# Kernel tuning notes

Measured on AMD Instinct MI355X. Metric: run time of the kernel, lower is better.

Reference implementation:

```python
import jax, jax.numpy as jnp
import numpy as np

EPS = 1e-8
N_ITER = 3
S = 8      # n_slots
D = 64     # slot_size
HID = 128  # mlp hidden


def _ln(x, w, b):
    m = jnp.mean(x, axis=-1, keepdims=True)
    v = jnp.var(x, axis=-1, keepdims=True)
    return (x - m) * jax.lax.rsqrt(v + 1e-5) * w + b


def setup_inputs() -> dict:
    key = jax.random.key(0)
    ks = jax.random.split(key, 20)
    B, N, Din = 128, 4096, 64
    g = lambda k, sh, s: (jax.random.normal(k, sh, jnp.float32) * s)
    return {
        "inputs": jax.random.normal(ks[0], (B, N, Din), jnp.float32),
        "eps_noise": jax.random.normal(ks[1], (B, S, D), jnp.float32),
        "slot_mu": g(ks[2], (1, 1, D), 0.1),
        "slot_logvar": g(ks[3], (1, 1, D), 0.1),
        "k_w": g(ks[4], (D, Din), 1.0 / np.sqrt(Din)),
        "v_w": g(ks[5], (D, Din), 1.0 / np.sqrt(Din)),
        "q_w": g(ks[6], (D, D), 1.0 / np.sqrt(D)),
        "ni_w": jnp.ones((Din,), jnp.float32), "ni_b": jnp.zeros((Din,), jnp.float32),
        "ns_w": jnp.ones((D,), jnp.float32),  "ns_b": jnp.zeros((D,), jnp.float32),
        "nr_w": jnp.ones((D,), jnp.float32),  "nr_b": jnp.zeros((D,), jnp.float32),
        "gru_wih": g(ks[7], (3 * D, D), 1.0 / np.sqrt(D)),
        "gru_whh": g(ks[8], (3 * D, D), 1.0 / np.sqrt(D)),
        "gru_bih": jnp.zeros((3 * D,), jnp.float32),
        "gru_bhh": jnp.zeros((3 * D,), jnp.float32),
        "mlp_w1": g(ks[9], (HID, D), 1.0 / np.sqrt(D)),
        "mlp_w2": g(ks[10], (D, HID), 1.0 / np.sqrt(HID)),
        "mlp_b2": jnp.zeros((D,), jnp.float32),
    }


def _gru(x, h, wih, whh, bih, bhh):
    gi = x @ wih.T + bih  # [BS, 3D]
    gh = h @ whh.T + bhh
    i_r, i_z, i_n = jnp.split(gi, 3, axis=-1)
    h_r, h_z, h_n = jnp.split(gh, 3, axis=-1)
    r = jax.nn.sigmoid(i_r + h_r)
    z = jax.nn.sigmoid(i_z + h_z)
    n = jnp.tanh(i_n + r * h_n)
    return (1.0 - z) * n + z * h


def _step(slots, k, v, q_w, ns_w, ns_b, nr_w, nr_b,
          gru_wih, gru_whh, gru_bih, gru_bhh, mlp_w1, mlp_w2, mlp_b2):
    B = slots.shape[0]
    q = _ln(slots, ns_w, ns_b) @ q_w.T                     # [B,S,D]
    logits = jnp.einsum('bnd,bsd->bns', k, q)              # [B,N,S]
    w = jax.nn.softmax(logits, axis=-1) + EPS              # softmax over slots
    w = w / jnp.sum(w, axis=-2, keepdims=True)             # renorm over tokens
    atten_maps = jnp.einsum('bns,bnd->bsd', w, v)          # [B,S,D]
    h = _gru(atten_maps.reshape(B * S, D), slots.reshape(B * S, D),
             gru_wih, gru_whh, gru_bih, gru_bhh)
    h = h + (jax.nn.relu(_ln(h, nr_w, nr_b) @ mlp_w1.T) @ mlp_w2.T + mlp_b2)
    return h.reshape(B, S, D), w


def reference(inputs, eps_noise, slot_mu, slot_logvar, k_w, v_w, q_w,
              ni_w, ni_b, ns_w, ns_b, nr_w, nr_b,
              gru_wih, gru_whh, gru_bih, gru_bhh, mlp_w1, mlp_w2, mlp_b2):
    std = jnp.exp(0.5 * slot_logvar)
    slots = slot_mu + std * eps_noise                      # [B,S,D]
    x = _ln(inputs, ni_w, ni_b)
    k = (x @ k_w.T) / np.sqrt(D).astype(np.float32)        # [B,N,D]
    v = x @ v_w.T
    args = (q_w, ns_w, ns_b, nr_w, nr_b, gru_wih, gru_whh,
            gru_bih, gru_bhh, mlp_w1, mlp_w2, mlp_b2)
    for _ in range(N_ITER):
        slots, w = _step(slots, k, v, *args)
    slots, w = _step(jax.lax.stop_gradient(slots), k, v, *args)
    return slots, w
```

## Files before the change

### kernel.cpp

```cpp
#include <hip/hip_runtime.h>
#include <hip/hip_bf16.h>

#define BB 128
#define NN 4096
#define DD 64
#define SS 8
#define HH 128

typedef __attribute__((ext_vector_type(8))) short short8;
typedef __attribute__((ext_vector_type(4))) float f32x4;

__device__ __forceinline__ float warp_red_sum(float v) {
    #pragma unroll
    for (int off = 32; off; off >>= 1) v += __shfl_xor(v, off);
    return v;
}

__device__ __forceinline__ float bcastlane(float v, int l) {
    return __int_as_float(__builtin_amdgcn_readlane(__float_as_int(v), l));
}

__device__ __forceinline__ unsigned short bfu(float f) {
    __hip_bfloat16 h = __float2bfloat16(f);
    return *(unsigned short*)&h;
}

__device__ __forceinline__ unsigned pk2(float a, float b) {
    return (unsigned)bfu(a) | ((unsigned)bfu(b) << 16);
}

__global__ __launch_bounds__(256) void prep_kernel(
    const float* __restrict__ v_w, const float* __restrict__ q_w,
    const float* __restrict__ wih, const float* __restrict__ whh,
    const float* __restrict__ w1, const float* __restrict__ w2,
    float* __restrict__ vwT, float* __restrict__ qwT,
    float* __restrict__ wihT, float* __restrict__ whhT,
    float* __restrict__ w1T, float* __restrict__ w2T)
{
    int i0 = blockIdx.x * blockDim.x + threadIdx.x;
    int nthr = gridDim.x * blockDim.x;
    for (int t = i0; t < 4096; t += nthr) {
        int i = t >> 6, o = t & 63;
        vwT[t] = v_w[o * 64 + i];
        qwT[t] = q_w[o * 64 + i];
    }
    for (int t = i0; t < 12288; t += nthr) {
        int r = t / 192, c = t % 192;
        wihT[t] = wih[c * 64 + r];
        whhT[t] = whh[c * 64 + r];
    }
    for (int t = i0; t < 8192; t += nthr) {
        int r = t >> 7, c = t & 127;
        w1T[t] = w1[c * 64 + r];
    }
    for (int t = i0; t < 8192; t += nthr) {
        int r = t >> 6, c = t & 63;
        w2T[t] = w2[c * 128 + r];
    }
}

__global__ __launch_bounds__(256) void init_q_kernel(
    const float* __restrict__ eps, const float* __restrict__ mu,
    const float* __restrict__ lv, const float* __restrict__ qwT,
    const float* __restrict__ k_w,
    const float* __restrict__ nsw, const float* __restrict__ nsb,
    float* __restrict__ slots, unsigned short* __restrict__ qb,
    float* __restrict__ zbuf)
{
    const int tid = threadIdx.x, lane = tid & 63;
    const int row = blockIdx.x * 4 + (tid >> 6);
    const int idx = row * 64 + lane;
    float s0 = mu[lane] + __expf(0.5f * lv[lane]) * eps[idx];
    slots[idx] = s0;
    float m = warp_red_sum(s0) * (1.0f / 64.0f);
    float dx = s0 - m;
    float var = warp_red_sum(dx * dx) * (1.0f / 64.0f);
    float xln = dx * rsqrtf(var + 1e-5f) * nsw[lane] + nsb[lane];
    float q = 0.f;
    #pragma unroll 8
    for (int i = 0; i < 64; ++i) q = fmaf(bcastlane(xln, i), qwT[i * 64 + lane], q);
    float qp = 0.f;
    #pragma unroll 8
    for (int o = 0; o < 64; ++o) qp = fmaf(bcastlane(q, o), k_w[o * 64 + lane], qp);
    qb[idx] = bfu(qp * 0.125f);
    int g = blockIdx.x * 256 + tid;
    for (int j = g; j < 66560; j += 65536) zbuf[j] = 0.f;
}

__global__ __launch_bounds__(256) void phase_a_ln(
    const float* __restrict__ inp, const float* __restrict__ niw, const float* __restrict__ nib,
    unsigned short* __restrict__ xb, unsigned short* __restrict__ xbt)
{
    __shared__ unsigned short xt[64 * 136];
    const int tid = threadIdx.x, lane = tid & 63, widx = tid >> 6;
    const int t8 = lane >> 3, d8 = lane & 7;
    const float4 wn0 = *(const float4*)&niw[d8 * 8];
    const float4 wn1 = *(const float4*)&niw[d8 * 8 + 4];
    const float4 bn0 = *(const float4*)&nib[d8 * 8];
    const float4 bn1 = *(const float4*)&nib[d8 * 8 + 4];
    const int tok0 = blockIdx.x * 128;
    #pragma unroll
    for (int it = 0; it < 4; ++it) {
        const int m = widx * 32 + it * 8 + t8;
        const float* rowp = inp + (size_t)(tok0 + m) * 64 + d8 * 8;
        float4 a = *(const float4*)rowp;
        float4 c = *(const float4*)(rowp + 4);
        float s1 = (a.x + a.y + a.z + a.w) + (c.x + c.y + c.z + c.w);
        float s2 = fmaf(a.x, a.x, fmaf(a.y, a.y, fmaf(a.z, a.z, a.w * a.w)));
        s2 = fmaf(c.x, c.x, fmaf(c.y, c.y, fmaf(c.z, c.z, fmaf(c.w, c.w, s2))));
        #pragma unroll
        for (int o = 1; o < 8; o <<= 1) { s1 += __shfl_xor(s1, o); s2 += __shfl_xor(s2, o); }
        float mean = s1 * (1.0f / 64.0f);
        float var = s2 * (1.0f / 64.0f) - mean * mean;
        float rstd = rsqrtf(var + 1e-5f);
        float y[8];
        y[0] = (a.x - mean) * rstd * wn0.x + bn0.x;
        y[1] = (a.y - mean) * rstd * wn0.y + bn0.y;
        y[2] = (a.z - mean) * rstd * wn0.z + bn0.z;
        y[3] = (a.w - mean) * rstd * wn0.w + bn0.w;
        y[4] = (c.x - mean) * rstd * wn1.x + bn1.x;
        y[5] = (c.y - mean) * rstd * wn1.y + bn1.y;
        y[6] = (c.z - mean) * rstd * wn1.z + bn1.z;
        y[7] = (c.w - mean) * rstd * wn1.w + bn1.w;
        uint4 o4;
        o4.x = pk2(y[0], y[1]); o4.y = pk2(y[2], y[3]);
        o4.z = pk2(y[4], y[5]); o4.w = pk2(y[6], y[7]);
        *(uint4*)&xb[(size_t)(tok0 + m) * 64 + d8 * 8] = o4;
        const int mh = m >> 3, ml = m & 7;
        #pragma unroll
        for (int j = 0; j < 8; ++j) {
            const int d = d8 * 8 + j;
            const int col = (((mh ^ ((d >> 2) & 15)) << 3) | ml);
            xt[d * 136 + col] = bfu(y[j]);
        }
    }
    __syncthreads();
    const int b = blockIdx.x >> 5, tin = (blockIdx.x & 31) * 128;
    const int d = tid >> 2, q4 = tid & 3;
    const int sr = (d >> 2) & 15;
    #pragma unroll
    for (int c = 0; c < 4; ++c) {
        const int cc = q4 * 4 + c;
        uint4 o = *(uint4*)&xt[d * 136 + ((cc ^ sr) << 3)];
        *(uint4*)&xbt[((size_t)b * 64 + d) * 4096 + tin + cc * 8] = o;
    }
}

__global__ __launch_bounds__(256) void attn_mfma(
    const __hip_bfloat16* __restrict__ xb, const unsigned short* __restrict__ xbt,
    const unsigned short* __restrict__ qb,
    float* __restrict__ numer, float* __restrict__ denom, float* __restrict__ wout)
{
    __shared__ unsigned short smem[5760];
    unsigned short* Qs = smem;
    const int tid = threadIdx.x, lane = tid & 63, widx = tid >> 6;
    unsigned short* wls = smem + 1152 + widx * 1152;
    const int b = blockIdx.y;

    for (int t = tid; t < 1024; t += 256) {
        int s = t >> 6, dd = t & 63;
        Qs[s * 72 + dd] = (s < 8) ? qb[b * 512 + t] : (unsigned short)0;
    }
    for (int t = lane; t < 576; t += 64) wls[576 + t] = 0;
    __syncthreads();

    const int quad = lane >> 4, l16 = lane & 15;
    short8 aq0 = *(const short8*)&Qs[l16 * 72 + quad * 8];
    short8 aq1 = *(const short8*)&Qs[l16 * 72 + 32 + quad * 8];

    f32x4 accv[4];
    #pragma unroll
    for (int nt = 0; nt < 4; ++nt) accv[nt] = (f32x4){0.f, 0.f, 0.f, 0.f};
    float dacc[4] = {0.f, 0.f, 0.f, 0.f};

    const int twave0 = blockIdx.x * 512 + widx * 128;
    #pragma unroll
    for (int iter = 0; iter < 2; ++iter) {
        const int t0 = twave0 + iter * 64;
        short8 bvr[8];
        #pragma unroll
        for (int ks = 0; ks < 2; ++ks)
            #pragma unroll
            for (int nt = 0; nt < 4; ++nt)
                bvr[ks * 4 + nt] = *(const short8*)&xbt[((size_t)b * 64 + nt * 16 + l16) * 4096
                                                        + t0 + ks * 32 + quad * 8];

        #pragma unroll
        for (int t4 = 0; t4 < 4; ++t4) {
            const int tok = t0 + t4 * 16 + l16;
            const size_t xrow = ((size_t)b * NN + tok) * 64;
            short8 bk0 = *(const short8*)&xb[xrow + quad * 8];
            short8 bk1 = *(const short8*)&xb[xrow + 32 + quad * 8];
            f32x4 lg = (f32x4){0.f, 0.f, 0.f, 0.f};
            lg = __builtin_amdgcn_mfma_f32_16x16x32_bf16(aq0, bk0, lg, 0, 0, 0);
            lg = __builtin_amdgcn_mfma_f32_16x16x32_bf16(aq1, bk1, lg, 0, 0, 0);
            float e[4];
            #pragma unroll
            for (int r = 0; r < 4; ++r) e[r] = __expf(lg[r]);
            float s4 = (e[0] + e[1]) + (e[2] + e[3]);
            float stot = s4 + __shfl_xor(s4, 16);
            float rs = __builtin_amdgcn_rcpf(stot);
            float wv[4];
            #pragma unroll
            for (int r = 0; r < 4; ++r) { wv[r] = fmaf(e[r], rs, 1e-8f); dacc[r] += wv[r]; }
            if (quad < 2) {
                #pragma unroll
                for (int r = 0; r < 4; ++r)
                    wls[(quad * 4 + r) * 72 + t4 * 16 + l16] = bfu(wv[r]);
                if (wout)
                    *(float4*)&wout[((size_t)b * NN + tok) * 8 + quad * 4] =
                        make_float4(wv[0], wv[1], wv[2], wv[3]);
            }
        }
        #pragma unroll
        for (int ks = 0; ks < 2; ++ks) {
            short8 aw = *(const short8*)&wls[l16 * 72 + ks * 32 + quad * 8];
            #pragma unroll
            for (int nt = 0; nt < 4; ++nt)
                accv[nt] = __builtin_amdgcn_mfma_f32_16x16x32_bf16(aw, bvr[ks * 4 + nt],
                                                                   accv[nt], 0, 0, 0);
        }
    }
    #pragma unroll
    for (int r = 0; r < 4; ++r) {
        dacc[r] += __shfl_xor(dacc[r], 1);
        dacc[r] += __shfl_xor(dacc[r], 2);
        dacc[r] += __shfl_xor(dacc[r], 4);
        dacc[r] += __shfl_xor(dacc[r], 8);
    }
    __syncthreads();
    float* red = (float*)smem;
    float* dred = red + 2048;
    if (quad < 2) {
        #pragma unroll
        for (int nt = 0; nt < 4; ++nt)
            #pragma unroll
            for (int r = 0; r < 4; ++r)
                red[widx * 512 + (quad * 4 + r) * 64 + nt * 16 + l16] = accv[nt][r];
        if (l16 == 0) {
            #pragma unroll
            for (int r = 0; r < 4; ++r) dred[widx * 8 + quad * 4 + r] = dacc[r];
        }
    }
    __syncthreads();
    for (int e = tid; e < 512; e += 256)
        atomicAdd(numer + (size_t)b * 512 + e, red[e] + red[512 + e] + red[1024 + e] + red[1536 + e]);
    if (tid < 8)
        atomicAdd(denom + b * 8 + tid, dred[tid] + dred[8 + tid] + dred[16 + tid] + dred[24 + tid]);
}

__global__ __launch_bounds__(256) void gru_q_kernel(
    const float* __restrict__ numerX, const float* __restrict__ denom,
    const float* __restrict__ slotsIn,
    const float* __restrict__ vwT, const float* __restrict__ wihT, const float* __restrict__ whhT,
    const float* __restrict__ w1T, const float* __restrict__ w2T,
    const float* __restrict__ bih, const float* __restrict__ bhh,
    const float* __restrict__ nrw, const float* __restrict__ nrb,
    const float* __restrict__ b2,
    const float* __restrict__ qwT, const float* __restrict__ k_w,
    const float* __restrict__ nsw, const float* __restrict__ nsb,
    float* __restrict__ slotsOut, unsigned short* __restrict__ qb,
    float* __restrict__ zbuf)
{
    const int tid = threadIdx.x, lane = tid & 63;
    const int row = blockIdx.x * 4 + (tid >> 6);
    float nx = numerX[row * 64 + lane];
    float xp = 0.f;
    #pragma unroll 8
    for (int i = 0; i < 64; ++i) xp = fmaf(bcastlane(nx, i), vwT[i * 64 + lane], xp);
    float x = xp / denom[row];
    float h = slotsIn[row * 64 + lane];
    float air = 0, aiz = 0, ain = 0, ahr = 0, ahz = 0, ahn = 0;
    #pragma unroll 8
    for (int i = 0; i < 64; ++i) {
        float xi = bcastlane(x, i), hi = bcastlane(h, i);
        const float* wi = wihT + i * 192;
        const float* wh = whhT + i * 192;
        air = fmaf(xi, wi[lane], air);
        aiz = fmaf(xi, wi[64 + lane], aiz);
        ain = fmaf(xi, wi[128 + lane], ain);
        ahr = fmaf(hi, wh[lane], ahr);
        ahz = fmaf(hi, wh[64 + lane], ahz);
        ahn = fmaf(hi, wh[128 + lane], ahn);
    }
    air += bih[lane]; aiz += bih[64 + lane]; ain += bih[128 + lane];
    ahr += bhh[lane]; ahz += bhh[64 + lane]; ahn += bhh[128 + lane];
    float r = 1.f / (1.f + __expf(-(air + ahr)));
    float z = 1.f / (1.f + __expf(-(aiz + ahz)));
    float n = tanhf(ain + r * ahn);
    float hn = (1.f - z) * n + z * h;
    float m = warp_red_sum(hn) * (1.0f / 64.0f);
    float dx = hn - m;
    float var = warp_red_sum(dx * dx) * (1.0f / 64.0f);
    float u = dx * rsqrtf(var + 1e-5f) * nrw[lane] + nrb[lane];
    float o0 = 0.f, o1 = 0.f;
    #pragma unroll 8
    for (int i = 0; i < 64; ++i) {
        float ui = bcastlane(u, i);
        const float* w1r = w1T + i * 128;
        o0 = fmaf(ui, w1r[lane], o0);
        o1 = fmaf(ui, w1r[64 + lane], o1);
    }
    o0 = fmaxf(o0, 0.f); o1 = fmaxf(o1, 0.f);
    float y = 0.f;
    #pragma unroll 8
    for (int j = 0; j < 64; ++j) y = fmaf(bcastlane(o0, j), w2T[j * 64 + lane], y);
    #pragma unroll 8
    for (int j = 0; j < 64; ++j) y = fmaf(bcastlane(o1, j), w2T[(64 + j) * 64 + lane], y);
    y += b2[lane];
    float out = hn + y;
    slotsOut[row * 64 + lane] = out;
    float m2 = warp_red_sum(out) * (1.0f / 64.0f);
    float dx2 = out - m2;
    float var2 = warp_red_sum(dx2 * dx2) * (1.0f / 64.0f);
    float u2 = dx2 * rsqrtf(var2 + 1e-5f) * nsw[lane] + nsb[lane];
    float q = 0.f;
    #pragma unroll 8
    for (int i = 0; i < 64; ++i) q = fmaf(bcastlane(u2, i), qwT[i * 64 + lane], q);
    float qp = 0.f;
    #pragma unroll 8
    for (int o = 0; o < 64; ++o) qp = fmaf(bcastlane(q, o), k_w[o * 64 + lane], qp);
    qb[row * 64 + lane] = bfu(qp * 0.125f);
    int g = blockIdx.x * 256 + tid;
    for (int j = g; j < 66560; j += 65536) zbuf[j] = 0.f;
}

__global__ __launch_bounds__(256) void renorm_kernel(float* __restrict__ wout,
                                                     const float* __restrict__ denom)
{
    const size_t i4 = (size_t)blockIdx.x * blockDim.x + threadIdx.x;
    const size_t b = i4 >> 13;
    const int half = (int)(i4 & 1);
    float4 v = reinterpret_cast<float4*>(wout)[i4];
    const float4 dv = reinterpret_cast<const float4*>(denom)[b * 2 + half];
    v.x /= dv.x; v.y /= dv.y; v.z /= dv.z; v.w /= dv.w;
    reinterpret_cast<float4*>(wout)[i4] = v;
}

extern "C" void kernel_launch(void* const* d_in, const int* in_sizes, int n_in,
                              void* d_out, int out_size, void* d_ws, size_t ws_size,
                              hipStream_t stream)
{
    const float* inputs  = (const float*)d_in[0];
    const float* eps_n   = (const float*)d_in[1];
    const float* mu      = (const float*)d_in[2];
    const float* lv      = (const float*)d_in[3];
    const float* k_w     = (const float*)d_in[4];
    const float* v_w     = (const float*)d_in[5];
    const float* q_w     = (const float*)d_in[6];
    const float* ni_w    = (const float*)d_in[7];
    const float* ni_b    = (const float*)d_in[8];
    const float* ns_w    = (const float*)d_in[9];
    const float* ns_b    = (const float*)d_in[10];
    const float* nr_w    = (const float*)d_in[11];
    const float* nr_b    = (const float*)d_in[12];
    const float* gru_wih = (const float*)d_in[13];
    const float* gru_whh = (const float*)d_in[14];
    const float* gru_bih = (const float*)d_in[15];
    const float* gru_bhh = (const float*)d_in[16];
    const float* mlp_w1  = (const float*)d_in[17];
    const float* mlp_w2  = (const float*)d_in[18];
    const float* mlp_b2  = (const float*)d_in[19];

    char* wsb = (char*)d_ws;
    unsigned short* xb  = (unsigned short*)wsb;
    unsigned short* xbt = (unsigned short*)(wsb + 67108864);
    float* f      = (float*)(wsb + 134217728);
    float* slotsA = f;
    float* slotsB = f + 65536;
    unsigned short* qb = (unsigned short*)(f + 131072);
    float* numer0 = f + 163840;
    float* denom0 = f + 229376;
    float* numer1 = f + 230400;
    float* denom1 = f + 295936;
    float* vwT    = f + 296960;
    float* qwT    = f + 301056;
    float* wihT   = f + 305152;
    float* whhT   = f + 317440;
    float* w1T    = f + 329728;
    float* w2T    = f + 337920;

    float* out_slots = (float*)d_out;
    float* out_w     = out_slots + 65536;

    prep_kernel<<<64, 256, 0, stream>>>(v_w, q_w, gru_wih, gru_whh, mlp_w1, mlp_w2,
                                        vwT, qwT, wihT, whhT, w1T, w2T);
    init_q_kernel<<<256, 256, 0, stream>>>(eps_n, mu, lv, qwT, k_w, ns_w, ns_b,
                                           slotsA, qb, numer0);
    phase_a_ln<<<4096, 256, 0, stream>>>(inputs, ni_w, ni_b, xb, xbt);

    float* cur = slotsA;
    float* numers[2] = {numer0, numer1};
    float* denoms[2] = {denom0, denom1};
    for (int step = 0; step < 4; ++step) {
        int pb = step & 1;
        attn_mfma<<<dim3(8, 128), 256, 0, stream>>>((const __hip_bfloat16*)xb, xbt, qb,
                                                    numers[pb], denoms[pb],
                                                    step == 3 ? out_w : nullptr);
        float* nxt = (step == 3) ? out_slots : ((step & 1) ? slotsA : slotsB);
        gru_q_kernel<<<256, 256, 0, stream>>>(numers[pb], denoms[pb], cur,
                                              vwT, wihT, whhT, w1T, w2T,
                                              gru_bih, gru_bhh, nr_w, nr_b, mlp_b2,
                                              qwT, k_w, ns_w, ns_b,
                                              nxt, qb, numers[1 - pb]);
        cur = nxt;
    }
    renorm_kernel<<<4096, 256, 0, stream>>>(out_w, denom1);
}
```

Baseline: 446.0 us.

## Drop global transposed activation copy; transpose per-wave tiles in LDS inside attention

Removes the second, transposed bf16 copy of the normalized inputs that phase_a_ln wrote and attention read every iteration. Instead each wave scatters its loaded token rows into a private LDS tile and reads them back transposed as MFMA B operands for the weighted-sum GEMM. This cuts a large global write plus repeated global reads per step. In exchange it adds many scalar LDS stores and extra LDS footprint per block, which may lower occupancy or cause bank conflicts.

```diff
diff --git a/kernel.cpp b/kernel.cpp
--- a/kernel.cpp
+++ b/kernel.cpp
@@ -8,6 +8,7 @@
 #define HH 128
 
 typedef __attribute__((ext_vector_type(8))) short short8;
+typedef __attribute__((ext_vector_type(4))) short short4v;
 typedef __attribute__((ext_vector_type(4))) float f32x4;
 
 __device__ __forceinline__ float warp_red_sum(float v) {
@@ -89,9 +90,8 @@
 
 __global__ __launch_bounds__(256) void phase_a_ln(
     const float* __restrict__ inp, const float* __restrict__ niw, const float* __restrict__ nib,
-    unsigned short* __restrict__ xb, unsigned short* __restrict__ xbt)
-{
-    __shared__ unsigned short xt[64 * 136];
+    unsigned short* __restrict__ xb)
+{
     const int tid = threadIdx.x, lane = tid & 63, widx = tid >> 6;
     const int t8 = lane >> 3, d8 = lane & 7;
     const float4 wn0 = *(const float4*)&niw[d8 * 8];
@@ -126,35 +126,19 @@
         o4.x = pk2(y[0], y[1]); o4.y = pk2(y[2], y[3]);
         o4.z = pk2(y[4], y[5]); o4.w = pk2(y[6], y[7]);
         *(uint4*)&xb[(size_t)(tok0 + m) * 64 + d8 * 8] = o4;
-        const int mh = m >> 3, ml = m & 7;
-        #pragma unroll
-        for (int j = 0; j < 8; ++j) {
-            const int d = d8 * 8 + j;
-            const int col = (((mh ^ ((d >> 2) & 15)) << 3) | ml);
-            xt[d * 136 + col] = bfu(y[j]);
-        }
-    }
-    __syncthreads();
-    const int b = blockIdx.x >> 5, tin = (blockIdx.x & 31) * 128;
-    const int d = tid >> 2, q4 = tid & 3;
-    const int sr = (d >> 2) & 15;
-    #pragma unroll
-    for (int c = 0; c < 4; ++c) {
-        const int cc = q4 * 4 + c;
-        uint4 o = *(uint4*)&xt[d * 136 + ((cc ^ sr) << 3)];
-        *(uint4*)&xbt[((size_t)b * 64 + d) * 4096 + tin + cc * 8] = o;
     }
 }
 
 __global__ __launch_bounds__(256) void attn_mfma(
-    const __hip_bfloat16* __restrict__ xb, const unsigned short* __restrict__ xbt,
+    const __hip_bfloat16* __restrict__ xb,
     const unsigned short* __restrict__ qb,
     float* __restrict__ numer, float* __restrict__ denom, float* __restrict__ wout)
 {
-    __shared__ unsigned short smem[5760];
+    __shared__ unsigned short smem[14976];
     unsigned short* Qs = smem;
     const int tid = threadIdx.x, lane = tid & 63, widx = tid >> 6;
     unsigned short* wls = smem + 1152 + widx * 1152;
+    unsigned short* Xw  = smem + 5760 + widx * 2304;
     const int b = blockIdx.y;
 
     for (int t = tid; t < 1024; t += 256) {
@@ -177,48 +161,59 @@
     #pragma unroll
     for (int iter = 0; iter < 2; ++iter) {
         const int t0 = twave0 + iter * 64;
-        short8 bvr[8];
-        #pragma unroll
-        for (int ks = 0; ks < 2; ++ks)
-            #pragma unroll
-            for (int nt = 0; nt < 4; ++nt)
-                bvr[ks * 4 + nt] = *(const short8*)&xbt[((size_t)b * 64 + nt * 16 + l16) * 4096
-                                                        + t0 + ks * 32 + quad * 8];
-
+        short8 bk[4][2];
         #pragma unroll
         for (int t4 = 0; t4 < 4; ++t4) {
-            const int tok = t0 + t4 * 16 + l16;
-            const size_t xrow = ((size_t)b * NN + tok) * 64;
-            short8 bk0 = *(const short8*)&xb[xrow + quad * 8];
-            short8 bk1 = *(const short8*)&xb[xrow + 32 + quad * 8];
-            f32x4 lg = (f32x4){0.f, 0.f, 0.f, 0.f};
-            lg = __builtin_amdgcn_mfma_f32_16x16x32_bf16(aq0, bk0, lg, 0, 0, 0);
-            lg = __builtin_amdgcn_mfma_f32_16x16x32_bf16(aq1, bk1, lg, 0, 0, 0);
-            float e[4];
-            #pragma unroll
-            for (int r = 0; r < 4; ++r) e[r] = __expf(lg[r]);
-            float s4 = (e[0] + e[1]) + (e[2] + e[3]);
-            float stot = s4 + __shfl_xor(s4, 16);
-            float rs = __builtin_amdgcn_rcpf(stot);
-            float wv[4];
-            #pragma unroll
-            for (int r = 0; r < 4; ++r) { wv[r] = fmaf(e[r], rs, 1e-8f); dacc[r] += wv[r]; }
-            if (quad < 2) {
-                #pragma unroll
-                for (int r = 0; r < 4; ++r)
-                    wls[(quad * 4 + r) * 72 + t4 * 16 + l16] = bfu(wv[r]);
-                if (wout)
-                    *(float4*)&wout[((size_t)b * NN + tok) * 8 + quad * 4] =
-                        make_float4(wv[0], wv[1], wv[2], wv[3]);
-            }
+            const size_t xrow = ((size_t)b * NN + t0 + t4 * 16 + l16) * 64;
+            bk[t4][0] = *(const short8*)&xb[xrow + quad * 8];
+            bk[t4][1] = *(const short8*)&xb[xrow + 32 + quad * 8];
         }
         #pragma unroll
-        for (int ks = 0; ks < 2; ++ks) {
-            short8 aw = *(const short8*)&wls[l16 * 72 + ks * 32 + quad * 8];
+        for (int h = 0; h < 2; ++h) {
             #pragma unroll
-            for (int nt = 0; nt < 4; ++nt)
-                accv[nt] = __builtin_amdgcn_mfma_f32_16x16x32_bf16(aw, bvr[ks * 4 + nt],
-                                                                   accv[nt], 0, 0, 0);
+            for (int t4h = 0; t4h < 2; ++t4h) {
+                const int t4 = h * 2 + t4h;
+                const int tok = t0 + t4 * 16 + l16;
+                const int tl = t4h * 16 + l16;
+                short8 bk0 = bk[t4][0];
+                short8 bk1 = bk[t4][1];
+                #pragma unroll
+                for (int j = 0; j < 8; ++j) {
+                    Xw[(quad * 8 + j) * 36 + tl]      = (unsigned short)bk0[j];
+                    Xw[(32 + quad * 8 + j) * 36 + tl] = (unsigned short)bk1[j];
+                }
+                f32x4 lg = (f32x4){0.f, 0.f, 0.f, 0.f};
+                lg = __builtin_amdgcn_mfma_f32_16x16x32_bf16(aq0, bk0, lg, 0, 0, 0);
+                lg = __builtin_amdgcn_mfma_f32_16x16x32_bf16(aq1, bk1, lg, 0, 0, 0);
+                float e[4];
+                #pragma unroll
+                for (int r = 0; r < 4; ++r) e[r] = __expf(lg[r]);
+                float s4 = (e[0] + e[1]) + (e[2] + e[3]);
+                float stot = s4 + __shfl_xor(s4, 16);
+                float rs = __builtin_amdgcn_rcpf(stot);
+                float wv[4];
+                #pragma unroll
+                for (int r = 0; r < 4; ++r) { wv[r] = fmaf(e[r], rs, 1e-8f); dacc[r] += wv[r]; }
+                if (quad < 2) {
+                    #pragma unroll
+                    for (int r = 0; r < 4; ++r)
+                        wls[(quad * 4 + r) * 72 + t4 * 16 + l16] = bfu(wv[r]);
+                    if (wout)
+                        *(float4*)&wout[((size_t)b * NN + tok) * 8 + quad * 4] =
+                            make_float4(wv[0], wv[1], wv[2], wv[3]);
+                }
+            }
+            short8 aw = *(const short8*)&wls[l16 * 72 + h * 32 + quad * 8];
+            #pragma unroll
+            for (int nt = 0; nt < 4; ++nt) {
+                const unsigned short* Xr = Xw + (nt * 16 + l16) * 36 + quad * 8;
+                short4v lo = *(const short4v*)Xr;
+                short4v hi = *(const short4v*)(Xr + 4);
+                short8 bv;
+                bv[0] = lo[0]; bv[1] = lo[1]; bv[2] = lo[2]; bv[3] = lo[3];
+                bv[4] = hi[0]; bv[5] = hi[1]; bv[6] = hi[2]; bv[7] = hi[3];
+                accv[nt] = __builtin_amdgcn_mfma_f32_16x16x32_bf16(aw, bv, accv[nt], 0, 0, 0);
+            }
         }
     }
     #pragma unroll
@@ -364,7 +359,6 @@
 
     char* wsb = (char*)d_ws;
     unsigned short* xb  = (unsigned short*)wsb;
-    unsigned short* xbt = (unsigned short*)(wsb + 67108864);
     float* f      = (float*)(wsb + 134217728);
     float* slotsA = f;
     float* slotsB = f + 65536;
@@ -387,14 +381,14 @@
                                         vwT, qwT, wihT, whhT, w1T, w2T);
     init_q_kernel<<<256, 256, 0, stream>>>(eps_n, mu, lv, qwT, k_w, ns_w, ns_b,
                                            slotsA, qb, numer0);
-    phase_a_ln<<<4096, 256, 0, stream>>>(inputs, ni_w, ni_b, xb, xbt);
+    phase_a_ln<<<4096, 256, 0, stream>>>(inputs, ni_w, ni_b, xb);
 
     float* cur = slotsA;
     float* numers[2] = {numer0, numer1};
     float* denoms[2] = {denom0, denom1};
     for (int step = 0; step < 4; ++step) {
         int pb = step & 1;
-        attn_mfma<<<dim3(8, 128), 256, 0, stream>>>((const __hip_bfloat16*)xb, xbt, qb,
+        attn_mfma<<<dim3(8, 128), 256, 0, stream>>>((const __hip_bfloat16*)xb, qb,
                                                     numers[pb], denoms[pb],
                                                     step == 3 ? out_w : nullptr);
         float* nxt = (step == 3) ? out_slots : ((step & 1) ? slotsA : slotsB);
```

Measured after the change: 392.8 us. 11.9% less time.
